# Performance work log

Measured on AMD Instinct MI355X. Metric: run time of the kernel, lower is better.

## Reference

```python
import jax, jax.numpy as jnp
import numpy as np

B, C, H, W, K = 4, 64, 128, 128, 3
K2 = K * K
PAD = (K - 1) // 2  # same padding for 3x3


def setup_inputs() -> dict:
    key = jax.random.key(0)
    ks = jax.random.split(key, 9)
    s = 0.05
    return {
        "x": jax.random.normal(ks[0], (B, C, H, W), jnp.float32),
        "inter": jax.random.normal(ks[1], (B, C, H, W), jnp.float32),
        # offset/mask predictor conv: input cat([x, inter]) -> 3*K2 channels (dy, dx, mask)
        "w_offset": jax.random.normal(ks[2], (3 * K2, 2 * C, K, K), jnp.float32) * s,
        "b_offset": jnp.zeros((3 * K2,), jnp.float32),
        # deformable conv weight (bias=False per DGM init)
        "w_dcn": jax.random.normal(ks[3], (C, C, K, K), jnp.float32) * s,
        # SFT gamma branch: two 1x1 convs (bias=False)
        "w_g1": jax.random.normal(ks[4], (C, C), jnp.float32) * s,
        "w_g2": jax.random.normal(ks[5], (C, C), jnp.float32) * s,
        # SFT beta branch: two 1x1 convs (bias=False)
        "w_b1": jax.random.normal(ks[6], (C, C), jnp.float32) * s,
        "w_b2": jax.random.normal(ks[7], (C, C), jnp.float32) * s,
    }


def _lrelu(v):
    # LeakyReLU(0.1)
    return jnp.where(v >= 0, v, 0.1 * v)


def _conv(x, w, b=None):
    y = jax.lax.conv_general_dilated(
        x, w, window_strides=(1, 1), padding=[(PAD, PAD), (PAD, PAD)],
        dimension_numbers=("NCHW", "OIHW", "NCHW"))
    if b is not None:
        y = y + b[None, :, None, None]
    return y


def _bilinear_gather(x, py, px):
    """x: [B,C,H,W]; py, px: [B,K2,H,W] float sample coords.
    Returns samples [B,K2,H,W,C]; out-of-bounds treated as zero (DCN zero-pad)."""
    y0 = jnp.floor(py)
    x0 = jnp.floor(px)
    wy = (py - y0)[..., None]
    wx = (px - x0)[..., None]

    def gather(yi, xi):
        valid = ((yi >= 0) & (yi < H) & (xi >= 0) & (xi < W)).astype(x.dtype)
        yc = jnp.clip(yi, 0, H - 1).astype(jnp.int32)
        xc = jnp.clip(xi, 0, W - 1).astype(jnp.int32)
        bidx = jnp.arange(B)[:, None, None, None]
        v = x[bidx, :, yc, xc]  # advanced indexing -> [B,K2,H,W,C]
        return v * valid[..., None]

    v00 = gather(y0, x0)
    v01 = gather(y0, x0 + 1)
    v10 = gather(y0 + 1, x0)
    v11 = gather(y0 + 1, x0 + 1)
    return (v00 * (1 - wy) * (1 - wx) + v01 * (1 - wy) * wx
            + v10 * wy * (1 - wx) + v11 * wy * wx)


def _dgm_forward(x, inter, w_offset, b_offset, w_dcn, w_g1, w_g2, w_b1, w_b2):
    # --- WADCN branch: modulated deformable conv, offsets predicted from cat(x, inter)
    om = _conv(jnp.concatenate([x, inter], axis=1), w_offset, b_offset)  # [B,3K2,H,W]
    dy, dx, m = jnp.split(om, 3, axis=1)  # each [B,K2,H,W]
    mask = jax.nn.sigmoid(m)

    ky, kx = jnp.meshgrid(jnp.arange(K), jnp.arange(K), indexing="ij")
    ky = ky.reshape(K2).astype(x.dtype)
    kx = kx.reshape(K2).astype(x.dtype)
    hh = jnp.arange(H, dtype=x.dtype)
    ww = jnp.arange(W, dtype=x.dtype)
    # sample coords: base grid + kernel-tap offset + learned offset
    py = hh[None, None, :, None] + (ky - PAD)[None, :, None, None] + dy  # [B,K2,H,W]
    px = ww[None, None, None, :] + (kx - PAD)[None, :, None, None] + dx

    samp = _bilinear_gather(x, py, px) * mask[..., None]  # [B,K2,H,W,C]
    dcn_out = jnp.einsum("bkhwc,ock->bohw", samp, w_dcn.reshape(C, C, K2))

    # --- SFT branch: two 1x1-conv + LeakyReLU chains producing gamma/beta
    gamma = jnp.einsum("oc,bchw->bohw", w_g2,
                       _lrelu(jnp.einsum("oc,bchw->bohw", w_g1, inter)))
    beta = jnp.einsum("oc,bchw->bohw", w_b2,
                      _lrelu(jnp.einsum("oc,bchw->bohw", w_b1, inter)))
    sft_out = x * gamma + beta

    # --- fused residual combine (DGM.relu is defined but never applied)
    return x + dcn_out + sft_out


def reference(x, inter, w_offset, b_offset, w_dcn, w_g1, w_g2, w_b1, w_b2):
    return _dgm_forward(x, inter, w_offset, b_offset, w_dcn, w_g1, w_g2, w_b1, w_b2)
```

## Files before the change

### kernel.cpp

```cpp
#include <hip/hip_runtime.h>
#include <hip/hip_bf16.h>
#include <math.h>

#define BB 4
#define CC 64
#define HH 128
#define WW 128
#define HW (HH*WW)
#define NPIX (BB*HW)

typedef __attribute__((ext_vector_type(8))) short short8;
typedef __attribute__((ext_vector_type(4))) float f32x4;

__device__ __forceinline__ float bf2f(ushort u) {
  union { unsigned u; float f; } v; v.u = ((unsigned)u) << 16; return v.f;
}
__device__ __forceinline__ ushort f2bf(float f) {
  __hip_bfloat16 h = __float2bfloat16(f); return *(ushort*)&h;
}

__global__ __launch_bounds__(256) void k_prep(
    const float* __restrict__ x, const float* __restrict__ inter,
    const float* __restrict__ w_off, const float* __restrict__ w_dcn,
    const float* __restrict__ wg1, const float* __restrict__ wb1,
    const float* __restrict__ wg2, const float* __restrict__ wb2,
    ushort* __restrict__ x_clh, ushort* __restrict__ inter_clh,
    ushort* __restrict__ wfb, ushort* __restrict__ wdT,
    ushort* __restrict__ w1gb, ushort* __restrict__ w1bb,
    ushort* __restrict__ w2gb, ushort* __restrict__ w2bb,
    float* __restrict__ zp) {
  __shared__ float tile[64 * 129];
  int blk = blockIdx.x;
  if (blk < 1024) {
    int sel = blk >> 9;
    int bh = blk & 511;
    int b = bh >> 7, h = bh & 127;
    const float* src = sel ? inter : x;
    ushort* dst = sel ? inter_clh : x_clh;
    const float* sp = src + (size_t)(b * 64) * HW + h * WW;
    for (int i = threadIdx.x; i < 64 * 128; i += 256) {
      int c = i >> 7, w = i & 127;
      tile[c * 129 + w] = sp[(size_t)c * HW + w];
    }
    __syncthreads();
    ushort* dp = dst + ((size_t)b * HW + h * WW) * 64;
    for (int i = threadIdx.x; i < 64 * 128; i += 256) {
      int w = i >> 6, c = i & 63;
      dp[w * 64 + c] = f2bf(tile[c * 129 + w]);
    }
  } else if (blk < 1168) {
    int i = (blk - 1024) * 256 + threadIdx.x;
    if (i < 64) zp[i] = 0.f;
    if (i < 9 * 32 * 128) {
      int tap = i >> 12, rem = i & 4095, m = rem >> 7, c = rem & 127;
      float v = (m < 27) ? w_off[(size_t)(m * 128 + c) * 9 + tap] : 0.f;
      wfb[i] = f2bf(v);
    }
  } else if (blk < 1312) {
    int i = (blk - 1168) * 256 + threadIdx.x;
    if (i < 64 * 64 * 9) {
      int o = i / 576, rem = i % 576, k = rem >> 6, c = rem & 63;
      wdT[i] = f2bf(w_dcn[(o * 64 + c) * 9 + k]);
    }
  } else {
    int i = (blk - 1312) * 256 + threadIdx.x;
    int m = i >> 12, j = i & 4095;
    const float* src = (m == 0) ? wg1 : (m == 1) ? wb1 : (m == 2) ? wg2 : wb2;
    ushort* dst = (m == 0) ? w1gb : (m == 1) ? w1bb : (m == 2) ? w2gb : w2bb;
    dst[j] = f2bf(src[j]);
  }
}

#define CPITCH 72

__global__ __launch_bounds__(256) void k_convm(
    const ushort* __restrict__ x_clh, const ushort* __restrict__ inter_clh,
    const ushort* __restrict__ wfb, float* __restrict__ om) {
  __shared__ ushort S[6 * 34 * CPITCH];
  int tid = threadIdx.x;
  int wave = tid >> 6, lane = tid & 63;
  int quad = lane >> 4, col = lane & 15;
  int blk = blockIdx.x;
  int b = blk >> 9, h = (blk >> 2) & 127, wq = blk & 3;
  int pt = wave >> 1, mt = wave & 1;

  {
    int ch = (tid & 7) * 8;
    unsigned bbase = (unsigned)b * HW;
#pragma unroll
    for (int it = 0; it < 7; ++it) {
      int e = it * 32 + (tid >> 3);
      if (e < 204) {
        int srcrow = e / 34, pxl = e % 34;
        int src = srcrow / 3, row = srcrow % 3;
        int hs = h + row - 1;
        int ps = wq * 32 + pxl - 1;
        bool ok = ((unsigned)hs < 128u) && ((unsigned)ps < 128u);
        int hc = hs < 0 ? 0 : (hs > 127 ? 127 : hs);
        int pc = ps < 0 ? 0 : (ps > 127 ? 127 : ps);
        const ushort* sb = src ? inter_clh : x_clh;
        short8 v = *(const short8*)(sb + ((size_t)(bbase + (hc << 7) + pc)) * 64 + ch);
        short8 z = {0, 0, 0, 0, 0, 0, 0, 0};
        if (!ok) v = z;
        *(short8*)(&S[e * CPITCH + ch]) = v;
      }
    }
  }
  __syncthreads();

  f32x4 accx = {0.f, 0.f, 0.f, 0.f}, acci = {0.f, 0.f, 0.f, 0.f};
  const ushort* wb0 = wfb + (size_t)(mt * 16 + col) * 128 + quad * 8;
  int pxb = pt * 16 + col;

#pragma unroll
  for (int ky = 0; ky < 3; ++ky) {
#pragma unroll
    for (int kx = 0; kx < 3; ++kx) {
      int tap = ky * 3 + kx;
      const ushort* wt = wb0 + (size_t)tap * 4096;
#pragma unroll
      for (int ks = 0; ks < 2; ++ks) {
        short8 a0 = *(const short8*)(wt + ks * 32);
        short8 b0 = *(const short8*)(&S[(ky * 34 + pxb + kx) * CPITCH + ks * 32 + quad * 8]);
        accx = __builtin_amdgcn_mfma_f32_16x16x32_bf16(a0, b0, accx, 0, 0, 0);
        short8 a1 = *(const short8*)(wt + 64 + ks * 32);
        short8 b1 = *(const short8*)(&S[((3 + ky) * 34 + pxb + kx) * CPITCH + ks * 32 + quad * 8]);
        acci = __builtin_amdgcn_mfma_f32_16x16x32_bf16(a1, b1, acci, 0, 0, 0);
      }
    }
  }

  int pg = b * HW + h * WW + wq * 32 + pt * 16 + col;
#pragma unroll
  for (int r = 0; r < 4; ++r) {
    int o = mt * 16 + quad * 4 + r;
    float v = accx[r] + acci[r];
    if (o < 27) om[(size_t)o * NPIX + pg] = v;
  }
}

#define SPITCH 200
#define NPX 32
#define FP32 72

__global__ __launch_bounds__(256) void k_mega(
    const float* __restrict__ x, const ushort* __restrict__ x_clh,
    const ushort* __restrict__ inter_clh, const float* __restrict__ om,
    const float* __restrict__ b_off, const ushort* __restrict__ wdT,
    const ushort* __restrict__ w1gb, const ushort* __restrict__ w1bb,
    const ushort* __restrict__ w2gb, const ushort* __restrict__ w2bb,
    const ushort* __restrict__ zp16, float* __restrict__ out) {
  __shared__ ushort S[NPX * SPITCH];
  __shared__ __align__(16) char U[2 * NPX * FP32 * 2];
  ushort* Sg = (ushort*)U;
  ushort* Sb = Sg + NPX * FP32;
  int*   cy  = (int*)U;
  int*   cx  = cy + 288;
  float* cwy = (float*)(cx + 288);
  float* cwx = cwy + 288;
  float* cm  = cwx + 288;

  int tid = threadIdx.x;
  int wave = tid >> 6, lane = tid & 63;
  int quad = lane >> 4, col = lane & 15;
  int rr = lane >> 3, g = lane & 7;
  int pg0 = blockIdx.x * NPX;
  int b = pg0 >> 14, hw0 = pg0 & 16383;
  int o_base = __builtin_amdgcn_readfirstlane(wave * 16);

  f32x4 ag[2], ab[2];
#pragma unroll
  for (int nt = 0; nt < 2; ++nt) {
    ag[nt] = (f32x4){0.f, 0.f, 0.f, 0.f};
    ab[nt] = (f32x4){0.f, 0.f, 0.f, 0.f};
  }
#pragma unroll
  for (int ks = 0; ks < 2; ++ks) {
    short8 a_g = *(const short8*)(w1gb + (size_t)(o_base + col) * 64 + ks * 32 + quad * 8);
    short8 a_b = *(const short8*)(w1bb + (size_t)(o_base + col) * 64 + ks * 32 + quad * 8);
#pragma unroll
    for (int nt = 0; nt < 2; ++nt) {
      short8 bf = *(const short8*)(inter_clh + (size_t)(pg0 + nt * 16 + col) * 64 + ks * 32 + quad * 8);
      ag[nt] = __builtin_amdgcn_mfma_f32_16x16x32_bf16(a_g, bf, ag[nt], 0, 0, 0);
      ab[nt] = __builtin_amdgcn_mfma_f32_16x16x32_bf16(a_b, bf, ab[nt], 0, 0, 0);
    }
  }
#pragma unroll
  for (int nt = 0; nt < 2; ++nt) {
    int px = nt * 16 + col;
    ushort pkg[4], pkb[4];
#pragma unroll
    for (int r = 0; r < 4; ++r) {
      float vg = ag[nt][r]; vg = vg >= 0.f ? vg : 0.1f * vg;
      float vb = ab[nt][r]; vb = vb >= 0.f ? vb : 0.1f * vb;
      pkg[r] = f2bf(vg); pkb[r] = f2bf(vb);
    }
    *(uint2*)(&Sg[px * FP32 + o_base + quad * 4]) = *(uint2*)pkg;
    *(uint2*)(&Sb[px * FP32 + o_base + quad * 4]) = *(uint2*)pkb;
  }
  __syncthreads();

  f32x4 gg[2], gb[2];
#pragma unroll
  for (int nt = 0; nt < 2; ++nt) {
    gg[nt] = (f32x4){0.f, 0.f, 0.f, 0.f};
    gb[nt] = (f32x4){0.f, 0.f, 0.f, 0.f};
  }
#pragma unroll
  for (int ks = 0; ks < 2; ++ks) {
    short8 a_g = *(const short8*)(w2gb + (size_t)(o_base + col) * 64 + ks * 32 + quad * 8);
    short8 a_b = *(const short8*)(w2bb + (size_t)(o_base + col) * 64 + ks * 32 + quad * 8);
#pragma unroll
    for (int nt = 0; nt < 2; ++nt) {
      short8 bgf = *(const short8*)(Sg + (nt * 16 + col) * FP32 + ks * 32 + quad * 8);
      short8 bbf = *(const short8*)(Sb + (nt * 16 + col) * FP32 + ks * 32 + quad * 8);
      gg[nt] = __builtin_amdgcn_mfma_f32_16x16x32_bf16(a_g, bgf, gg[nt], 0, 0, 0);
      gb[nt] = __builtin_amdgcn_mfma_f32_16x16x32_bf16(a_b, bbf, gb[nt], 0, 0, 0);
    }
  }
  __syncthreads();

  for (int i = tid; i < 9 * NPX; i += 256) {
    int k = i >> 5, p = i & 31;
    int pg = pg0 + p;
    int hw = pg & 16383;
    int h = hw >> 7, w = hw & 127;
    float dy = om[(size_t)k * NPIX + pg] + b_off[k];
    float dx = om[(size_t)(9 + k) * NPIX + pg] + b_off[9 + k];
    float mz = om[(size_t)(18 + k) * NPIX + pg] + b_off[18 + k];
    float py = (float)(h + (k / 3) - 1) + dy;
    float px = (float)(w + (k % 3) - 1) + dx;
    float y0f = floorf(py), x0f = floorf(px);
    cy[i] = (int)y0f;
    cx[i] = (int)x0f;
    cwy[i] = py - y0f;
    cwx[i] = px - x0f;
    cm[i] = 1.f / (1.f + __expf(-mz));
  }

  f32x4 acc[2];
  acc[0] = (f32x4){0.f, 0.f, 0.f, 0.f};
  acc[1] = (f32x4){0.f, 0.f, 0.f, 0.f};

  const ushort* bp = x_clh + (size_t)b * HW * 64;

  for (int chunk = 0; chunk < 3; ++chunk) {
    __syncthreads();
#pragma unroll
    for (int it = 0; it < 3; ++it) {
      int p = wave * 8 + rr;
      int idx = (chunk * 3 + it) * NPX + p;
      int y0 = cy[idx], x0 = cx[idx];
      float wy = cwy[idx], wx = cwx[idx], m = cm[idx];
      bool yok0 = (unsigned)y0 < 128u, yok1 = (unsigned)(y0 + 1) < 128u;
      bool xok0 = (unsigned)x0 < 128u, xok1 = (unsigned)(x0 + 1) < 128u;
      const ushort* r0 = bp + ((size_t)(int)((y0 << 7) + x0)) * 64 + g * 8;
      const ushort* r1 = r0 + (size_t)WW * 64;
      short8 s00 = *(const short8*)((yok0 && xok0) ? r0 : zp16);
      short8 s01 = *(const short8*)((yok0 && xok1) ? (r0 + 64) : zp16);
      short8 s10 = *(const short8*)((yok1 && xok0) ? r1 : zp16);
      short8 s11 = *(const short8*)((yok1 && xok1) ? (r1 + 64) : zp16);
      short8 outv;
#pragma unroll
      for (int j = 0; j < 8; ++j) {
        float v00 = bf2f((ushort)s00[j]), v01 = bf2f((ushort)s01[j]);
        float v10 = bf2f((ushort)s10[j]), v11 = bf2f((ushort)s11[j]);
        float top = v00 + (v01 - v00) * wx;
        float bot = v10 + (v11 - v10) * wx;
        float val = top + (bot - top) * wy;
        outv[j] = (short)f2bf(val * m);
      }
      *(short8*)(&S[p * SPITCH + it * 64 + g * 8]) = outv;
    }
    __syncthreads();
    const ushort* wrow = wdT + (size_t)(o_base + col) * 576 + chunk * 192 + quad * 8;
    const ushort* srow = S + quad * 8;
#pragma unroll
    for (int ks = 0; ks < 6; ++ks) {
      short8 a = *(const short8*)(wrow + ks * 32);
#pragma unroll
      for (int nt = 0; nt < 2; ++nt) {
        short8 bf = *(const short8*)(srow + (nt * 16 + col) * SPITCH + ks * 32);
        acc[nt] = __builtin_amdgcn_mfma_f32_16x16x32_bf16(a, bf, acc[nt], 0, 0, 0);
      }
    }
  }

#pragma unroll
  for (int nt = 0; nt < 2; ++nt) {
#pragma unroll
    for (int r = 0; r < 4; ++r) {
      int o = o_base + quad * 4 + r;
      size_t idx = (size_t)(b * 64 + o) * HW + hw0 + nt * 16 + col;
      float xv = x[idx];
      out[idx] = xv + xv * gg[nt][r] + gb[nt][r] + acc[nt][r];
    }
  }
}

extern "C" void kernel_launch(void* const* d_in, const int* in_sizes, int n_in,
                              void* d_out, int out_size, void* d_ws, size_t ws_size,
                              hipStream_t stream) {
  const float* x     = (const float*)d_in[0];
  const float* inter = (const float*)d_in[1];
  const float* w_off = (const float*)d_in[2];
  const float* b_off = (const float*)d_in[3];
  const float* w_dcn = (const float*)d_in[4];
  const float* wg1   = (const float*)d_in[5];
  const float* wg2   = (const float*)d_in[6];
  const float* wb1   = (const float*)d_in[7];
  const float* wb2   = (const float*)d_in[8];
  float* out = (float*)d_out;

  float* ws        = (float*)d_ws;
  ushort* x_clh    = (ushort*)ws;
  ushort* inter_clh= (ushort*)(ws + 2097152);
  float* om        = ws + 4194304;
  ushort* wfb      = (ushort*)(ws + 5963776);
  ushort* wdT      = (ushort*)(ws + 5982208);
  ushort* w1gb     = (ushort*)(ws + 6000640);
  ushort* w1bb     = (ushort*)(ws + 6002688);
  ushort* w2gb     = (ushort*)(ws + 6004736);
  ushort* w2bb     = (ushort*)(ws + 6006784);
  float* zp        = ws + 6008832;

  k_prep<<<1376, 256, 0, stream>>>(x, inter, w_off, w_dcn, wg1, wb1, wg2, wb2,
                                   x_clh, inter_clh, wfb, wdT,
                                   w1gb, w1bb, w2gb, w2bb, zp);

  k_convm<<<2048, 256, 0, stream>>>(x_clh, inter_clh, wfb, om);

  k_mega<<<2048, 256, 0, stream>>>(x, x_clh, inter_clh, om, b_off, wdT,
                                   w1gb, w1bb, w2gb, w2bb,
                                   (const ushort*)zp, out);
}
```

Before: 178.4 us.

## Fuse offset/mask conv into the deformable-conv megakernel via shared memory

The separate offset/mask convolution kernel is merged into the main deformable-conv kernel. Each block now computes its 27 offset/mask channels for its 32 pixels into LDS instead of writing them to a global buffer, which removes one launch and the global write and read of the offset map. Both kernels already tiled 32 pixels per block, so the mapping lines up. Shared-memory regions are aliased across phases to limit LDS growth. The x residual load is also hoisted earlier, which costs more registers and adds extra syncs.

```diff
diff --git a/kernel.cpp b/kernel.cpp
--- a/kernel.cpp
+++ b/kernel.cpp
@@ -72,17 +72,38 @@
 }
 
 #define CPITCH 72
-
-__global__ __launch_bounds__(256) void k_convm(
-    const ushort* __restrict__ x_clh, const ushort* __restrict__ inter_clh,
-    const ushort* __restrict__ wfb, float* __restrict__ om) {
-  __shared__ ushort S[6 * 34 * CPITCH];
+#define SPITCH 200
+#define NPX 32
+#define FPX 72
+
+__global__ __launch_bounds__(256) void k_omega(
+    const float* __restrict__ x, const ushort* __restrict__ x_clh,
+    const ushort* __restrict__ inter_clh,
+    const float* __restrict__ b_off, const ushort* __restrict__ wfb,
+    const ushort* __restrict__ wdT,
+    const ushort* __restrict__ w1gb, const ushort* __restrict__ w1bb,
+    const ushort* __restrict__ w2gb, const ushort* __restrict__ w2bb,
+    const ushort* __restrict__ zp16, float* __restrict__ out) {
+  __shared__ __align__(16) ushort BIGB[6 * 34 * CPITCH];
+  __shared__ float oml[28 * 33];
+  ushort* S  = BIGB;
+  ushort* Sg = BIGB + 6400;
+  ushort* Sb = Sg + NPX * FPX;
+  int*   cy  = (int*)(BIGB + 6400);
+  int*   cx  = cy + 288;
+  float* cwy = (float*)(cx + 288);
+  float* cwx = cwy + 288;
+  float* cm  = cwx + 288;
+
   int tid = threadIdx.x;
   int wave = tid >> 6, lane = tid & 63;
   int quad = lane >> 4, col = lane & 15;
-  int blk = blockIdx.x;
-  int b = blk >> 9, h = (blk >> 2) & 127, wq = blk & 3;
+  int rr = lane >> 3, g = lane & 7;
+  int pg0 = blockIdx.x * NPX;
+  int b = pg0 >> 14, hw0 = pg0 & 16383;
+  int h = hw0 >> 7, w0 = hw0 & 127;
   int pt = wave >> 1, mt = wave & 1;
+  int o_base = __builtin_amdgcn_readfirstlane(wave * 16);
 
   {
     int ch = (tid & 7) * 8;
@@ -94,7 +115,7 @@
         int srcrow = e / 34, pxl = e % 34;
         int src = srcrow / 3, row = srcrow % 3;
         int hs = h + row - 1;
-        int ps = wq * 32 + pxl - 1;
+        int ps = w0 + pxl - 1;
         bool ok = ((unsigned)hs < 128u) && ((unsigned)ps < 128u);
         int hc = hs < 0 ? 0 : (hs > 127 ? 127 : hs);
         int pc = ps < 0 ? 0 : (ps > 127 ? 127 : ps);
@@ -102,71 +123,40 @@
         short8 v = *(const short8*)(sb + ((size_t)(bbase + (hc << 7) + pc)) * 64 + ch);
         short8 z = {0, 0, 0, 0, 0, 0, 0, 0};
         if (!ok) v = z;
-        *(short8*)(&S[e * CPITCH + ch]) = v;
+        *(short8*)(&BIGB[e * CPITCH + ch]) = v;
       }
     }
   }
   __syncthreads();
 
-  f32x4 accx = {0.f, 0.f, 0.f, 0.f}, acci = {0.f, 0.f, 0.f, 0.f};
-  const ushort* wb0 = wfb + (size_t)(mt * 16 + col) * 128 + quad * 8;
-  int pxb = pt * 16 + col;
-
-#pragma unroll
-  for (int ky = 0; ky < 3; ++ky) {
-#pragma unroll
-    for (int kx = 0; kx < 3; ++kx) {
-      int tap = ky * 3 + kx;
-      const ushort* wt = wb0 + (size_t)tap * 4096;
-#pragma unroll
-      for (int ks = 0; ks < 2; ++ks) {
-        short8 a0 = *(const short8*)(wt + ks * 32);
-        short8 b0 = *(const short8*)(&S[(ky * 34 + pxb + kx) * CPITCH + ks * 32 + quad * 8]);
-        accx = __builtin_amdgcn_mfma_f32_16x16x32_bf16(a0, b0, accx, 0, 0, 0);
-        short8 a1 = *(const short8*)(wt + 64 + ks * 32);
-        short8 b1 = *(const short8*)(&S[((3 + ky) * 34 + pxb + kx) * CPITCH + ks * 32 + quad * 8]);
-        acci = __builtin_amdgcn_mfma_f32_16x16x32_bf16(a1, b1, acci, 0, 0, 0);
+  {
+    f32x4 accx = {0.f, 0.f, 0.f, 0.f}, acci = {0.f, 0.f, 0.f, 0.f};
+    const ushort* wb0 = wfb + (size_t)(mt * 16 + col) * 128 + quad * 8;
+    int pxb = pt * 16 + col;
+#pragma unroll
+    for (int ky = 0; ky < 3; ++ky) {
+#pragma unroll
+      for (int kx = 0; kx < 3; ++kx) {
+        int tap = ky * 3 + kx;
+        const ushort* wt = wb0 + (size_t)tap * 4096;
+#pragma unroll
+        for (int ks = 0; ks < 2; ++ks) {
+          short8 a0 = *(const short8*)(wt + ks * 32);
+          short8 b0 = *(const short8*)(&BIGB[(ky * 34 + pxb + kx) * CPITCH + ks * 32 + quad * 8]);
+          accx = __builtin_amdgcn_mfma_f32_16x16x32_bf16(a0, b0, accx, 0, 0, 0);
+          short8 a1 = *(const short8*)(wt + 64 + ks * 32);
+          short8 b1 = *(const short8*)(&BIGB[((3 + ky) * 34 + pxb + kx) * CPITCH + ks * 32 + quad * 8]);
+          acci = __builtin_amdgcn_mfma_f32_16x16x32_bf16(a1, b1, acci, 0, 0, 0);
+        }
       }
     }
-  }
-
-  int pg = b * HW + h * WW + wq * 32 + pt * 16 + col;
-#pragma unroll
-  for (int r = 0; r < 4; ++r) {
-    int o = mt * 16 + quad * 4 + r;
-    float v = accx[r] + acci[r];
-    if (o < 27) om[(size_t)o * NPIX + pg] = v;
-  }
-}
-
-#define SPITCH 200
-#define NPX 32
-#define FP32 72
-
-__global__ __launch_bounds__(256) void k_mega(
-    const float* __restrict__ x, const ushort* __restrict__ x_clh,
-    const ushort* __restrict__ inter_clh, const float* __restrict__ om,
-    const float* __restrict__ b_off, const ushort* __restrict__ wdT,
-    const ushort* __restrict__ w1gb, const ushort* __restrict__ w1bb,
-    const ushort* __restrict__ w2gb, const ushort* __restrict__ w2bb,
-    const ushort* __restrict__ zp16, float* __restrict__ out) {
-  __shared__ ushort S[NPX * SPITCH];
-  __shared__ __align__(16) char U[2 * NPX * FP32 * 2];
-  ushort* Sg = (ushort*)U;
-  ushort* Sb = Sg + NPX * FP32;
-  int*   cy  = (int*)U;
-  int*   cx  = cy + 288;
-  float* cwy = (float*)(cx + 288);
-  float* cwx = cwy + 288;
-  float* cm  = cwx + 288;
-
-  int tid = threadIdx.x;
-  int wave = tid >> 6, lane = tid & 63;
-  int quad = lane >> 4, col = lane & 15;
-  int rr = lane >> 3, g = lane & 7;
-  int pg0 = blockIdx.x * NPX;
-  int b = pg0 >> 14, hw0 = pg0 & 16383;
-  int o_base = __builtin_amdgcn_readfirstlane(wave * 16);
+#pragma unroll
+    for (int r = 0; r < 4; ++r) {
+      int o = mt * 16 + quad * 4 + r;
+      if (o < 27) oml[o * 33 + pt * 16 + col] = accx[r] + acci[r];
+    }
+  }
+  __syncthreads();
 
   f32x4 ag[2], ab[2];
 #pragma unroll
@@ -195,8 +185,8 @@
       float vb = ab[nt][r]; vb = vb >= 0.f ? vb : 0.1f * vb;
       pkg[r] = f2bf(vg); pkb[r] = f2bf(vb);
     }
-    *(uint2*)(&Sg[px * FP32 + o_base + quad * 4]) = *(uint2*)pkg;
-    *(uint2*)(&Sb[px * FP32 + o_base + quad * 4]) = *(uint2*)pkb;
+    *(uint2*)(&Sg[px * FPX + o_base + quad * 4]) = *(uint2*)pkg;
+    *(uint2*)(&Sb[px * FPX + o_base + quad * 4]) = *(uint2*)pkb;
   }
   __syncthreads();
 
@@ -212,24 +202,29 @@
     short8 a_b = *(const short8*)(w2bb + (size_t)(o_base + col) * 64 + ks * 32 + quad * 8);
 #pragma unroll
     for (int nt = 0; nt < 2; ++nt) {
-      short8 bgf = *(const short8*)(Sg + (nt * 16 + col) * FP32 + ks * 32 + quad * 8);
-      short8 bbf = *(const short8*)(Sb + (nt * 16 + col) * FP32 + ks * 32 + quad * 8);
+      short8 bgf = *(const short8*)(Sg + (nt * 16 + col) * FPX + ks * 32 + quad * 8);
+      short8 bbf = *(const short8*)(Sb + (nt * 16 + col) * FPX + ks * 32 + quad * 8);
       gg[nt] = __builtin_amdgcn_mfma_f32_16x16x32_bf16(a_g, bgf, gg[nt], 0, 0, 0);
       gb[nt] = __builtin_amdgcn_mfma_f32_16x16x32_bf16(a_b, bbf, gb[nt], 0, 0, 0);
     }
   }
+  float xv[2][4];
+#pragma unroll
+  for (int nt = 0; nt < 2; ++nt)
+#pragma unroll
+    for (int r = 0; r < 4; ++r) {
+      int o = o_base + quad * 4 + r;
+      xv[nt][r] = x[(size_t)(b * 64 + o) * HW + hw0 + nt * 16 + col];
+    }
   __syncthreads();
 
   for (int i = tid; i < 9 * NPX; i += 256) {
     int k = i >> 5, p = i & 31;
-    int pg = pg0 + p;
-    int hw = pg & 16383;
-    int h = hw >> 7, w = hw & 127;
-    float dy = om[(size_t)k * NPIX + pg] + b_off[k];
-    float dx = om[(size_t)(9 + k) * NPIX + pg] + b_off[9 + k];
-    float mz = om[(size_t)(18 + k) * NPIX + pg] + b_off[18 + k];
+    float dy = oml[k * 33 + p] + b_off[k];
+    float dx = oml[(9 + k) * 33 + p] + b_off[9 + k];
+    float mz = oml[(18 + k) * 33 + p] + b_off[18 + k];
     float py = (float)(h + (k / 3) - 1) + dy;
-    float px = (float)(w + (k % 3) - 1) + dx;
+    float px = (float)(w0 + p + (k % 3) - 1) + dx;
     float y0f = floorf(py), x0f = floorf(px);
     cy[i] = (int)y0f;
     cx[i] = (int)x0f;
@@ -292,8 +287,7 @@
     for (int r = 0; r < 4; ++r) {
       int o = o_base + quad * 4 + r;
       size_t idx = (size_t)(b * 64 + o) * HW + hw0 + nt * 16 + col;
-      float xv = x[idx];
-      out[idx] = xv + xv * gg[nt][r] + gb[nt][r] + acc[nt][r];
+      out[idx] = xv[nt][r] + xv[nt][r] * gg[nt][r] + gb[nt][r] + acc[nt][r];
     }
   }
 }
@@ -315,7 +309,6 @@
   float* ws        = (float*)d_ws;
   ushort* x_clh    = (ushort*)ws;
   ushort* inter_clh= (ushort*)(ws + 2097152);
-  float* om        = ws + 4194304;
   ushort* wfb      = (ushort*)(ws + 5963776);
   ushort* wdT      = (ushort*)(ws + 5982208);
   ushort* w1gb     = (ushort*)(ws + 6000640);
@@ -328,9 +321,7 @@
                                    x_clh, inter_clh, wfb, wdT,
                                    w1gb, w1bb, w2gb, w2bb, zp);
 
-  k_convm<<<2048, 256, 0, stream>>>(x_clh, inter_clh, wfb, om);
-
-  k_mega<<<2048, 256, 0, stream>>>(x, x_clh, inter_clh, om, b_off, wdT,
-                                   w1gb, w1bb, w2gb, w2bb,
-                                   (const ushort*)zp, out);
-}
+  k_omega<<<2048, 256, 0, stream>>>(x, x_clh, inter_clh, b_off, wfb, wdT,
+                                    w1gb, w1bb, w2gb, w2bb,
+                                    (const ushort*)zp, out);
+}
```

Measured after the change: 172.1 us. 3.5% less time.
